# Kernel optimization log

Hardware: AMD Instinct MI355X
Metric: run time of the kernel (lower is better)

The kernel has to match this reference:

```python
import jax, jax.numpy as jnp
import numpy as np

DT = 0.01
THETA0 = 2.0   # OUParams.theta
SIGMA0 = 0.5   # OUParams.sigma
MU0 = 0.0      # OUParams.mu0
JUMP_RATE = 0.1
JUMP_SCALE = 0.2
ERP_WIDTH = 10.0

B, C, T = 16, 64, 1000
N_PATHS = 64


def setup_inputs() -> dict:
    key = jax.random.key(0)
    k_x, k_eps, k_jr, k_jm, k_jt = jax.random.split(key, 5)
    x = jax.random.normal(k_x, (B, C, T), dtype=jnp.float32)
    # learned scalar parameters (nn.Parameter initialized to 1.0)
    theta_scale = jnp.ones((), dtype=jnp.float32)
    sigma_scale = jnp.ones((), dtype=jnp.float32)
    # antithetic: only N_paths//2 independent normals
    eps = jax.random.normal(k_eps, (N_PATHS // 2, B, C, T), dtype=jnp.float32)
    jump_rand = jax.random.uniform(k_jr, (N_PATHS, B, C, 1), dtype=jnp.float32)
    jump_magnitude = jax.random.normal(k_jm, (N_PATHS, B, C, 1), dtype=jnp.float32)
    jump_times = jax.random.randint(k_jt, (N_PATHS, B, C, 1), T // 4, 3 * T // 4, dtype=jnp.int32)
    return {
        "x": x,
        "theta_scale": theta_scale,
        "sigma_scale": sigma_scale,
        "eps": eps,
        "jump_rand": jump_rand,
        "jump_magnitude": jump_magnitude,
        "jump_times": jump_times,
        "N_paths": N_PATHS,
    }


def reference(x, theta_scale, sigma_scale, eps, jump_rand, jump_magnitude, jump_times, N_paths):
    # Euler-Maruyama OU step (antithetic variates): paths = x + theta*(mu0-x)*dt + sqrt(dt)*eps*sigma
    theta = THETA0 * jnp.abs(theta_scale)
    sigma = SIGMA0 * jnp.abs(sigma_scale)
    eps_full = jnp.concatenate([eps, -eps], axis=0)            # [N, B, C, T]
    dW = jnp.sqrt(jnp.float32(DT)) * eps_full * sigma
    drift = theta * (MU0 - x[None]) * jnp.float32(DT)          # broadcast over N
    paths = x[None] + drift + dW                               # [N, B, C, T]
    # Vectorized ERP jump injection (replaces triple Python loop):
    T_len = x.shape[-1]
    t_grid = jnp.arange(T_len, dtype=jnp.float32)              # [T]
    # Gaussian ERP bump centered at jump_times, width 10 samples
    erp = jnp.exp(-0.5 * ((t_grid[None, None, None, :] - jump_times.astype(jnp.float32)) / ERP_WIDTH) ** 2)
    mask = (jump_rand < JUMP_RATE).astype(paths.dtype)          # [N, B, C, 1]
    paths = paths + mask * (JUMP_SCALE * jump_magnitude) * erp
    return paths
```

## Files before the change

### kernel.cpp

```cpp
#include <hip/hip_runtime.h>
#include <math.h>


#define DT_F 0.01f
#define THETA0 2.0f
#define SIGMA0 0.5f
#define JUMP_RATE 0.1f
#define JUMP_SCALE 0.2f
#define ERP_INV_W 0.1f

constexpr int B_ = 16;
constexpr int C_ = 64;
constexpr int T_ = 1000;
constexpr int NH_ = 32;
constexpr int BC_ = B_ * C_;
constexpr int CHUNKS_ = T_ / 4;
constexpr int NH_PER_BLK = 8;

__global__ __launch_bounds__(256) void eegsde_paths_kernel(
    const float* __restrict__ x,
    const float* __restrict__ theta_scale,
    const float* __restrict__ sigma_scale,
    const float* __restrict__ eps,
    const float* __restrict__ jump_rand,
    const float* __restrict__ jump_mag,
    const int*   __restrict__ jump_times,
    float* __restrict__ out)
{
    const int bc = blockIdx.x;
    const int tc = threadIdx.x;
    if (tc >= CHUNKS_) return;
    const int t0 = tc * 4;

    const float theta = THETA0 * fabsf(theta_scale[0]);
    const float sigma = SIGMA0 * fabsf(sigma_scale[0]);
    const float a  = 1.0f - theta * DT_F;
    const float sd = sqrtf(DT_F) * sigma;

    const float4 x4 = *reinterpret_cast<const float4*>(&x[bc * T_ + t0]);
    const float bx0 = a * x4.x;
    const float bx1 = a * x4.y;
    const float bx2 = a * x4.z;
    const float bx3 = a * x4.w;

    const float tf0 = (float)t0;
    const float tf1 = tf0 + 1.0f;
    const float tf2 = tf0 + 2.0f;
    const float tf3 = tf0 + 3.0f;

    const int nh_begin = blockIdx.y * NH_PER_BLK;
    const int nh_end   = nh_begin + NH_PER_BLK;

    #pragma unroll 2
    for (int nh = nh_begin; nh < nh_end; ++nh) {
        const int row = nh * BC_ + bc;
        const int jid0 = row;
        const int jid1 = (nh + NH_) * BC_ + bc;

        const float amp0 = (jump_rand[jid0] < JUMP_RATE) ? (JUMP_SCALE * jump_mag[jid0]) : 0.0f;
        const float amp1 = (jump_rand[jid1] < JUMP_RATE) ? (JUMP_SCALE * jump_mag[jid1]) : 0.0f;
        const float jt0 = (float)jump_times[jid0];
        const float jt1 = (float)jump_times[jid1];

        const float4 e4 = *reinterpret_cast<const float4*>(&eps[(size_t)row * T_ + t0]);

        const float dw0 = sd * e4.x;
        const float dw1 = sd * e4.y;
        const float dw2 = sd * e4.z;
        const float dw3 = sd * e4.w;

        const float d00 = (tf0 - jt0) * ERP_INV_W;
        const float d01 = (tf1 - jt0) * ERP_INV_W;
        const float d02 = (tf2 - jt0) * ERP_INV_W;
        const float d03 = (tf3 - jt0) * ERP_INV_W;
        const float d10 = (tf0 - jt1) * ERP_INV_W;
        const float d11 = (tf1 - jt1) * ERP_INV_W;
        const float d12 = (tf2 - jt1) * ERP_INV_W;
        const float d13 = (tf3 - jt1) * ERP_INV_W;

        const float j00 = amp0 * __expf(-0.5f * d00 * d00);
        const float j01 = amp0 * __expf(-0.5f * d01 * d01);
        const float j02 = amp0 * __expf(-0.5f * d02 * d02);
        const float j03 = amp0 * __expf(-0.5f * d03 * d03);
        const float j10 = amp1 * __expf(-0.5f * d10 * d10);
        const float j11 = amp1 * __expf(-0.5f * d11 * d11);
        const float j12 = amp1 * __expf(-0.5f * d12 * d12);
        const float j13 = amp1 * __expf(-0.5f * d13 * d13);

        float4 o0, o1;
        o0.x = bx0 + dw0 + j00;
        o0.y = bx1 + dw1 + j01;
        o0.z = bx2 + dw2 + j02;
        o0.w = bx3 + dw3 + j03;
        o1.x = bx0 - dw0 + j10;
        o1.y = bx1 - dw1 + j11;
        o1.z = bx2 - dw2 + j12;
        o1.w = bx3 - dw3 + j13;

        *reinterpret_cast<float4*>(&out[(size_t)row * T_ + t0]) = o0;
        *reinterpret_cast<float4*>(&out[(size_t)((nh + NH_) * BC_ + bc) * T_ + t0]) = o1;
    }
}

extern "C" void kernel_launch(void* const* d_in, const int* in_sizes, int n_in,
                              void* d_out, int out_size, void* d_ws, size_t ws_size,
                              hipStream_t stream) {
    const float* x           = (const float*)d_in[0];
    const float* theta_scale = (const float*)d_in[1];
    const float* sigma_scale = (const float*)d_in[2];
    const float* eps         = (const float*)d_in[3];
    const float* jump_rand   = (const float*)d_in[4];
    const float* jump_mag    = (const float*)d_in[5];
    const int*   jump_times  = (const int*)d_in[6];
    float* out = (float*)d_out;

    dim3 grid(BC_, NH_ / NH_PER_BLK, 1);
    dim3 block(256, 1, 1);
    eegsde_paths_kernel<<<grid, block, 0, stream>>>(
        x, theta_scale, sigma_scale, eps, jump_rand, jump_mag, jump_times, out);
}
```

Measured before the change: 82.87 us.

## Flatten work into a grid-stride loop and skip ERP math for unmasked rows

Replaces the per-(bc, path-group) 2D grid, in which six of 256 threads idle, with a flat grid-stride loop over all float4 chunks of the first path half, launched as 2048 blocks. The ERP exponentials and jump_times loads are skipped when neither antithetic path's jump mask is active, which holds for most rows. The point is to keep every lane busy and cut ALU work in a memory-bound kernel. The costs are a per-element integer divide and reloading x and the jump scalars for each chunk instead of once per row.

```diff
diff --git a/kernel.cpp b/kernel.cpp
--- a/kernel.cpp
+++ b/kernel.cpp
@@ -14,10 +14,14 @@
 constexpr int T_ = 1000;
 constexpr int NH_ = 32;
 constexpr int BC_ = B_ * C_;
-constexpr int CHUNKS_ = T_ / 4;
-constexpr int NH_PER_BLK = 8;
+constexpr uint32_t ROW4 = T_ / 4;
+constexpr uint32_t TOTAL4 = (uint32_t)NH_ * BC_ * ROW4;
+constexpr uint32_t HALF_ROWS = (uint32_t)NH_ * BC_;
+constexpr size_t   HALF_OFF_F = (size_t)HALF_ROWS * T_;
 
-__global__ __launch_bounds__(256) void eegsde_paths_kernel(
+typedef float f32x4 __attribute__((ext_vector_type(4)));
+
+__global__ __launch_bounds__(256, 8) void eegsde_paths_flat(
     const float* __restrict__ x,
     const float* __restrict__ theta_scale,
     const float* __restrict__ sigma_scale,
@@ -27,67 +31,61 @@
     const int*   __restrict__ jump_times,
     float* __restrict__ out)
 {
-    const int bc = blockIdx.x;
-    const int tc = threadIdx.x;
-    if (tc >= CHUNKS_) return;
-    const int t0 = tc * 4;
-
     const float theta = THETA0 * fabsf(theta_scale[0]);
     const float sigma = SIGMA0 * fabsf(sigma_scale[0]);
     const float a  = 1.0f - theta * DT_F;
     const float sd = sqrtf(DT_F) * sigma;
 
-    const float4 x4 = *reinterpret_cast<const float4*>(&x[bc * T_ + t0]);
-    const float bx0 = a * x4.x;
-    const float bx1 = a * x4.y;
-    const float bx2 = a * x4.z;
-    const float bx3 = a * x4.w;
+    const uint32_t stride = gridDim.x * blockDim.x;
+    uint32_t g = blockIdx.x * blockDim.x + threadIdx.x;
 
-    const float tf0 = (float)t0;
-    const float tf1 = tf0 + 1.0f;
-    const float tf2 = tf0 + 2.0f;
-    const float tf3 = tf0 + 3.0f;
+    for (; g < TOTAL4; g += stride) {
+        const uint32_t r  = g / ROW4;
+        const uint32_t tq = g - r * ROW4;
+        const uint32_t t0 = tq * 4u;
+        const uint32_t bc = r & (BC_ - 1);
+        const uint32_t r1 = r + HALF_ROWS;
 
-    const int nh_begin = blockIdx.y * NH_PER_BLK;
-    const int nh_end   = nh_begin + NH_PER_BLK;
+        const f32x4 e4 = *reinterpret_cast<const f32x4*>(&eps[(size_t)g * 4]);
+        const f32x4 x4 = *reinterpret_cast<const f32x4*>(&x[(size_t)bc * T_ + t0]);
 
-    #pragma unroll 2
-    for (int nh = nh_begin; nh < nh_end; ++nh) {
-        const int row = nh * BC_ + bc;
-        const int jid0 = row;
-        const int jid1 = (nh + NH_) * BC_ + bc;
-
-        const float amp0 = (jump_rand[jid0] < JUMP_RATE) ? (JUMP_SCALE * jump_mag[jid0]) : 0.0f;
-        const float amp1 = (jump_rand[jid1] < JUMP_RATE) ? (JUMP_SCALE * jump_mag[jid1]) : 0.0f;
-        const float jt0 = (float)jump_times[jid0];
-        const float jt1 = (float)jump_times[jid1];
-
-        const float4 e4 = *reinterpret_cast<const float4*>(&eps[(size_t)row * T_ + t0]);
+        const float amp0 = (jump_rand[r]  < JUMP_RATE) ? (JUMP_SCALE * jump_mag[r])  : 0.0f;
+        const float amp1 = (jump_rand[r1] < JUMP_RATE) ? (JUMP_SCALE * jump_mag[r1]) : 0.0f;
 
         const float dw0 = sd * e4.x;
         const float dw1 = sd * e4.y;
         const float dw2 = sd * e4.z;
         const float dw3 = sd * e4.w;
+        const float bx0 = a * x4.x;
+        const float bx1 = a * x4.y;
+        const float bx2 = a * x4.z;
+        const float bx3 = a * x4.w;
 
-        const float d00 = (tf0 - jt0) * ERP_INV_W;
-        const float d01 = (tf1 - jt0) * ERP_INV_W;
-        const float d02 = (tf2 - jt0) * ERP_INV_W;
-        const float d03 = (tf3 - jt0) * ERP_INV_W;
-        const float d10 = (tf0 - jt1) * ERP_INV_W;
-        const float d11 = (tf1 - jt1) * ERP_INV_W;
-        const float d12 = (tf2 - jt1) * ERP_INV_W;
-        const float d13 = (tf3 - jt1) * ERP_INV_W;
+        float j00 = 0.f, j01 = 0.f, j02 = 0.f, j03 = 0.f;
+        float j10 = 0.f, j11 = 0.f, j12 = 0.f, j13 = 0.f;
+        if ((amp0 != 0.0f) || (amp1 != 0.0f)) {
+            const float tf0 = (float)t0;
+            const float jt0 = (float)jump_times[r];
+            const float jt1 = (float)jump_times[r1];
+            const float d00 = (tf0        - jt0) * ERP_INV_W;
+            const float d01 = (tf0 + 1.f - jt0) * ERP_INV_W;
+            const float d02 = (tf0 + 2.f - jt0) * ERP_INV_W;
+            const float d03 = (tf0 + 3.f - jt0) * ERP_INV_W;
+            const float d10 = (tf0        - jt1) * ERP_INV_W;
+            const float d11 = (tf0 + 1.f - jt1) * ERP_INV_W;
+            const float d12 = (tf0 + 2.f - jt1) * ERP_INV_W;
+            const float d13 = (tf0 + 3.f - jt1) * ERP_INV_W;
+            j00 = amp0 * __expf(-0.5f * d00 * d00);
+            j01 = amp0 * __expf(-0.5f * d01 * d01);
+            j02 = amp0 * __expf(-0.5f * d02 * d02);
+            j03 = amp0 * __expf(-0.5f * d03 * d03);
+            j10 = amp1 * __expf(-0.5f * d10 * d10);
+            j11 = amp1 * __expf(-0.5f * d11 * d11);
+            j12 = amp1 * __expf(-0.5f * d12 * d12);
+            j13 = amp1 * __expf(-0.5f * d13 * d13);
+        }
 
-        const float j00 = amp0 * __expf(-0.5f * d00 * d00);
-        const float j01 = amp0 * __expf(-0.5f * d01 * d01);
-        const float j02 = amp0 * __expf(-0.5f * d02 * d02);
-        const float j03 = amp0 * __expf(-0.5f * d03 * d03);
-        const float j10 = amp1 * __expf(-0.5f * d10 * d10);
-        const float j11 = amp1 * __expf(-0.5f * d11 * d11);
-        const float j12 = amp1 * __expf(-0.5f * d12 * d12);
-        const float j13 = amp1 * __expf(-0.5f * d13 * d13);
-
-        float4 o0, o1;
+        f32x4 o0, o1;
         o0.x = bx0 + dw0 + j00;
         o0.y = bx1 + dw1 + j01;
         o0.z = bx2 + dw2 + j02;
@@ -97,8 +95,8 @@
         o1.z = bx2 - dw2 + j12;
         o1.w = bx3 - dw3 + j13;
 
-        *reinterpret_cast<float4*>(&out[(size_t)row * T_ + t0]) = o0;
-        *reinterpret_cast<float4*>(&out[(size_t)((nh + NH_) * BC_ + bc) * T_ + t0]) = o1;
+        *reinterpret_cast<f32x4*>(&out[(size_t)g * 4])               = o0;
+        *reinterpret_cast<f32x4*>(&out[(size_t)g * 4 + HALF_OFF_F])  = o1;
     }
 }
 
@@ -114,8 +112,8 @@
     const int*   jump_times  = (const int*)d_in[6];
     float* out = (float*)d_out;
 
-    dim3 grid(BC_, NH_ / NH_PER_BLK, 1);
+    dim3 grid(2048, 1, 1);
     dim3 block(256, 1, 1);
-    eegsde_paths_kernel<<<grid, block, 0, stream>>>(
+    eegsde_paths_flat<<<grid, block, 0, stream>>>(
         x, theta_scale, sigma_scale, eps, jump_rand, jump_mag, jump_times, out);
 }
```

New measurement: 86.13 us. 3.9% more time.
